# Optimization experiments

Measured on AMD Instinct MI355X. Metric: run time of the kernel, lower is better.

## Reference

```python
import jax, jax.numpy as jnp
import numpy as np

DIM = 256
HEADS = 8
KS = 3          # deform conv kernel size
N = KS * KS     # sampling points per output pixel
PAD = 1


def conv2d(x, w, b=None, stride=1, padding=0):
    out = jax.lax.conv_general_dilated(
        x, w, (stride, stride), [(padding, padding)] * 2,
        dimension_numbers=('NCHW', 'OIHW', 'NCHW'))
    if b is not None:
        out = out + b[None, :, None, None]
    return out


def deform_conv(x, w_pconv, b_pconv, w_dconv):
    b, c, h, w = x.shape
    offset = conv2d(x, w_pconv, b_pconv, padding=1)      # (b, 2N, h, w)
    off = offset.transpose(0, 2, 3, 1)                   # (b, h, w, 2N); [:N]=x-off, [N:]=y-off
    xp = jnp.pad(x, ((0, 0), (0, 0), (PAD, PAD), (PAD, PAD)))
    hp, wp = h + 2 * PAD, w + 2 * PAD
    r = jnp.arange(-(KS - 1) // 2, (KS - 1) // 2 + 1, dtype=x.dtype)
    pnx, pny = jnp.meshgrid(r, r, indexing='ij')
    # sampling positions, 1-indexed into the padded input (matches the torch ref)
    px = off[..., :N] + pnx.reshape(-1) + jnp.arange(1, h + 1, dtype=x.dtype)[None, :, None, None]
    py = off[..., N:] + pny.reshape(-1) + jnp.arange(1, w + 1, dtype=x.dtype)[None, None, :, None]
    fx = jnp.floor(px)
    fy = jnp.floor(py)
    qlt_x = jnp.clip(fx, 0, hp - 1)
    qlt_y = jnp.clip(fy, 0, wp - 1)
    qrb_x = jnp.clip(fx + 1, 0, hp - 1)
    qrb_y = jnp.clip(fy + 1, 0, wp - 1)
    pxc = jnp.clip(px, 0, hp - 1)
    pyc = jnp.clip(py, 0, wp - 1)
    # bilinear weights (can be negative at clamped borders, as in the torch ref)
    g_lt = (1 + (qlt_x - pxc)) * (1 + (qlt_y - pyc))
    g_rb = (1 - (qrb_x - pxc)) * (1 - (qrb_y - pyc))
    g_lb = (1 + (qlt_x - pxc)) * (1 - (qrb_y - pyc))
    g_rt = (1 - (qrb_x - pxc)) * (1 + (qlt_y - pyc))
    ilt_x = qlt_x.astype(jnp.int32)
    ilt_y = qlt_y.astype(jnp.int32)
    irb_x = qrb_x.astype(jnp.int32)
    irb_y = qrb_y.astype(jnp.int32)

    def gather(xb, ix, iy):
        return xb[:, ix, iy]                              # (c, h, w, N)

    gat = jax.vmap(gather)
    x_lt = gat(xp, ilt_x, ilt_y)
    x_rb = gat(xp, irb_x, irb_y)
    x_lb = gat(xp, ilt_x, irb_y)
    x_rt = gat(xp, irb_x, ilt_y)
    x_off = (g_lt[:, None] * x_lt + g_rb[:, None] * x_rb
             + g_lb[:, None] * x_lb + g_rt[:, None] * x_rt)   # (b, c, h, w, N)
    # 'b c h w (i j) -> b c (h i) (w j)' then ks-strided conv
    x_off = x_off.reshape(b, c, h, w, KS, KS).transpose(0, 1, 2, 4, 3, 5)
    x_off = x_off.reshape(b, c, h * KS, w * KS)
    return conv2d(x_off, w_dconv, None, stride=KS)


def ssa_forward(x, w_pconv, b_pconv, w_dconv, w_qkv, temperature, w_proj):
    b, c, h, w = x.shape
    hw = h * w
    ch = c // HEADS
    q = deform_conv(x, w_pconv, b_pconv, w_dconv)         # (b, c, h, w)
    qkv = jnp.einsum('bchw,oc->bohw', x, w_qkv)           # 1x1 conv, (b, 3c, h, w)
    k = qkv[:, c:2 * c]
    v = qkv[:, 2 * c:]
    q = q.reshape(b, HEADS, ch, hw)
    k = k.reshape(b, HEADS, ch, hw)
    v = v.reshape(b, HEADS, ch, hw)
    k = k / jnp.maximum(jnp.linalg.norm(k, axis=-1, keepdims=True), 1e-12)
    v = v / jnp.maximum(jnp.linalg.norm(v, axis=-1, keepdims=True), 1e-12)
    attn = jnp.einsum('bhcn,bhdn->bhcd', q, k) * temperature[None]   # (b, h, ch, ch)
    attn = jax.nn.softmax(attn, axis=-1)
    out = jnp.einsum('bhcd,bhdn->bhcn', attn, v).reshape(b, c, h, w)
    return jnp.einsum('bchw,oc->bohw', out, w_proj)       # project_out 1x1


def setup_inputs() -> dict:
    key = jax.random.key(0)
    ks = jax.random.split(key, 6)
    B, H, W = 2, 96, 96
    x = jax.random.normal(ks[0], (B, DIM, H, W), jnp.float32)
    w_pconv = jax.random.normal(ks[1], (2 * N, DIM, KS, KS), jnp.float32) * 0.01
    b_pconv = jax.random.normal(ks[2], (2 * N,), jnp.float32) * 0.01
    w_dconv = jax.random.normal(ks[3], (DIM, DIM, KS, KS), jnp.float32) * 0.02
    w_qkv = jax.random.normal(ks[4], (3 * DIM, DIM), jnp.float32) * 0.05
    temperature = jnp.ones((HEADS, 1, 1), jnp.float32)
    w_proj = jax.random.normal(ks[5], (DIM, DIM), jnp.float32) * 0.05
    return dict(x=x, w_pconv=w_pconv, b_pconv=b_pconv, w_dconv=w_dconv,
                w_qkv=w_qkv, temperature=temperature, w_proj=w_proj)


def reference(x, w_pconv, b_pconv, w_dconv, w_qkv, temperature, w_proj):
    return ssa_forward(x, w_pconv, b_pconv, w_dconv, w_qkv, temperature, w_proj)
```

## Files before the change

### kernel.cpp

```cpp
#include <hip/hip_runtime.h>
#include <math.h>

#define BB 2
#define CC 256
#define HW 96
#define PP 9216
#define KO 18
#define HEADS 8
#define NCH 36

typedef short bf16x8 __attribute__((ext_vector_type(8)));
typedef float f32x4 __attribute__((ext_vector_type(4)));

#define NP_O    0UL
#define IDX_O   331776UL
#define WGT_O   995328UL
#define WT2_O   1658880UL
#define WP2_O   2248704UL
#define WQ2_O   2322432UL
#define W2_O    2453504UL
#define QP_O    2584576UL
#define KV_O    12021760UL
#define INV_O   21458944UL
#define AP_O    21459968UL
#define AT_O    22049792UL

__device__ __forceinline__ ushort f2bf_rne(float f) {
    unsigned u = __float_as_uint(f);
    unsigned r = (u + 0x7FFFu + ((u >> 16) & 1u)) >> 16;
    return (ushort)r;
}
__device__ __forceinline__ float bf2f(ushort h) {
    return __uint_as_float(((unsigned)h) << 16);
}

__global__ __launch_bounds__(256) void k_prep_wt(const float* __restrict__ wd,
                                                 ushort* __restrict__ h,
                                                 ushort* __restrict__ lo) {
    int tid = blockIdx.x * 256 + threadIdx.x;
    if (tid >= 9 * 8 * 1024 * 8) return;
    int e = tid & 7;
    int u = (tid >> 3) & 1023;
    int cs = (tid >> 13) & 7;
    int kk = tid >> 16;
    int oh = u >> 6, rem = u & 63;
    int lrow = rem & 15, lhi = rem >> 4;
    int o = oh * 16 + lrow;
    int c = cs * 32 + lhi * 8 + e;
    float v = wd[o * 2304 + c * 9 + kk];
    ushort hh = f2bf_rne(v);
    h[tid] = hh;
    lo[tid] = f2bf_rne(v - bf2f(hh));
}

__global__ __launch_bounds__(256) void k_prep_wp(const float* __restrict__ wp,
                                                 ushort* __restrict__ h,
                                                 ushort* __restrict__ lo) {
    int tid = blockIdx.x * 256 + threadIdx.x;
    if (tid >= 9 * 8 * 128 * 8) return;
    int e = tid & 7;
    int u = (tid >> 3) & 127;
    int cs = (tid >> 10) & 7;
    int kk = tid >> 13;
    int mf = u >> 6, rem = u & 63;
    int lrow = rem & 15, lhi = rem >> 4;
    int o = mf * 16 + lrow;
    int c = cs * 32 + lhi * 8 + e;
    float v = (o < KO) ? wp[(o * 256 + c) * 9 + kk] : 0.f;
    ushort hh = f2bf_rne(v);
    h[tid] = hh;
    lo[tid] = f2bf_rne(v - bf2f(hh));
}

__global__ __launch_bounds__(256) void k_prep_w(const float* __restrict__ W,
                                                ushort* __restrict__ h,
                                                ushort* __restrict__ lo,
                                                int total) {
    int tid = blockIdx.x * 256 + threadIdx.x;
    if (tid >= total) return;
    int e = tid & 7;
    int u = (tid >> 3) & 1023;
    int csg = (tid >> 13) & 7;
    int mt = tid >> 16;
    int rem = u & 63;
    int lrow = rem & 15, lhi = rem >> 4;
    int o = mt * 256 + (u >> 6) * 16 + lrow;
    int c = csg * 32 + lhi * 8 + e;
    float v = W[o * 256 + c];
    ushort hh = f2bf_rne(v);
    h[tid] = hh;
    lo[tid] = f2bf_rne(v - bf2f(hh));
}

__global__ __launch_bounds__(256) void k_pconv(const float* __restrict__ x,
                                               const ushort* __restrict__ wp2h,
                                               const ushort* __restrict__ wp2l,
                                               float* __restrict__ ppart) {
    int s = blockIdx.x;
    int xcd = s & 7;
    int b = xcd & 1, ks = xcd >> 1;
    int p0 = (s >> 3) * 64;
    int t = threadIdx.x;
    int l = t & 63, w = t >> 6;
    int lrow = l & 15, lhi = l >> 4;
    int p = t & 63, cg = t >> 6;
    __shared__ __align__(16) ushort Sh[64 * 40];
    __shared__ __align__(16) ushort Sl[64 * 40];
    f32x4 acc[2];
    acc[0] = (f32x4)0.f; acc[1] = (f32x4)0.f;
    const float* xb = x + (size_t)b * CC * PP;
    int pix = p0 + p;
    int i_ = pix / 96, j_ = pix % 96;
#pragma unroll 1
    for (int cs = 0; cs < 2; ++cs) {
        int csg = ks * 2 + cs;
        const float* xc0 = xb + (size_t)(csg * 32 + cg * 8) * PP;
#pragma unroll 1
        for (int kk = 0; kk < 9; ++kk) {
            int di = kk / 3 - 1, dj = kk % 3 - 1;
            bool vOK = ((unsigned)(i_ + di) < 96u) && ((unsigned)(j_ + dj) < 96u);
            int poff = pix + di * 96 + dj;
            __syncthreads();
            bf16x8 ah[2], al[2];
#pragma unroll
            for (int mf = 0; mf < 2; ++mf) {
                size_t gi = (((size_t)(kk * 8 + csg)) * 128 + (mf * 64 + l)) * 8;
                ah[mf] = *(const bf16x8*)&wp2h[gi];
                al[mf] = *(const bf16x8*)&wp2l[gi];
            }
            bf16x8 vh, vl;
#pragma unroll
            for (int i = 0; i < 8; ++i) {
                float v = vOK ? xc0[(size_t)i * PP + poff] : 0.f;
                ushort hh = f2bf_rne(v);
                vh[i] = (short)hh;
                vl[i] = (short)f2bf_rne(v - bf2f(hh));
            }
            *(bf16x8*)&Sh[p * 40 + cg * 8] = vh;
            *(bf16x8*)&Sl[p * 40 + cg * 8] = vl;
            __syncthreads();
            bf16x8 Bh = *(const bf16x8*)&Sh[(w * 16 + lrow) * 40 + lhi * 8];
            bf16x8 Bl = *(const bf16x8*)&Sl[(w * 16 + lrow) * 40 + lhi * 8];
#pragma unroll
            for (int mf = 0; mf < 2; ++mf) {
                acc[mf] = __builtin_amdgcn_mfma_f32_16x16x32_bf16(ah[mf], Bh, acc[mf], 0, 0, 0);
                acc[mf] = __builtin_amdgcn_mfma_f32_16x16x32_bf16(ah[mf], Bl, acc[mf], 0, 0, 0);
                acc[mf] = __builtin_amdgcn_mfma_f32_16x16x32_bf16(al[mf], Bh, acc[mf], 0, 0, 0);
            }
        }
    }
    float* pr = ppart + ((size_t)(ks * BB + b) * 32) * PP;
#pragma unroll
    for (int mf = 0; mf < 2; ++mf)
#pragma unroll
        for (int j = 0; j < 4; ++j)
            pr[(size_t)(mf * 16 + lhi * 4 + j) * PP + p0 + w * 16 + lrow] = acc[mf][j];
}

__global__ __launch_bounds__(256) void k_bilin2(const float* __restrict__ pp,
                                                const float* __restrict__ bp,
                                                int4* __restrict__ idx4,
                                                float4* __restrict__ wgt4) {
    int idx = blockIdx.x * 256 + threadIdx.x;
    if (idx >= BB * 9 * PP) return;
    int p = idx % PP;
    int bn = idx / PP;
    int n = bn % 9, b = bn / 9;
    int i = p / 96, j = p % 96;
    float ox = bp[n], oy = bp[n + 9];
#pragma unroll
    for (int k = 0; k < 4; ++k) {
        ox += pp[((size_t)(k * BB + b) * 32 + n) * PP + p];
        oy += pp[((size_t)(k * BB + b) * 32 + n + 9) * PP + p];
    }
    float px = ox + (float)(n / 3 - 1) + (float)(i + 1);
    float py = oy + (float)(n % 3 - 1) + (float)(j + 1);
    float fx = floorf(px), fy = floorf(py);
    float qltx = fminf(fmaxf(fx, 0.f), 97.f);
    float qlty = fminf(fmaxf(fy, 0.f), 97.f);
    float qrbx = fminf(fmaxf(fx + 1.f, 0.f), 97.f);
    float qrby = fminf(fmaxf(fy + 1.f, 0.f), 97.f);
    float pxc = fminf(fmaxf(px, 0.f), 97.f);
    float pyc = fminf(fmaxf(py, 0.f), 97.f);
    float glt = (1.f + (qltx - pxc)) * (1.f + (qlty - pyc));
    float grb = (1.f - (qrbx - pxc)) * (1.f - (qrby - pyc));
    float glb = (1.f + (qltx - pxc)) * (1.f - (qrby - pyc));
    float grt = (1.f - (qrbx - pxc)) * (1.f + (qlty - pyc));
    int x0 = (int)qltx - 1, y0 = (int)qlty - 1;
    int x1 = (int)qrbx - 1, y1 = (int)qrby - 1;
    bool vlt = (x0 >= 0 && x0 < 96 && y0 >= 0 && y0 < 96);
    bool vrb = (x1 >= 0 && x1 < 96 && y1 >= 0 && y1 < 96);
    bool vlb = (x0 >= 0 && x0 < 96 && y1 >= 0 && y1 < 96);
    bool vrt = (x1 >= 0 && x1 < 96 && y0 >= 0 && y0 < 96);
    int4 id;
    id.x = vlt ? x0 * 96 + y0 : 0;
    id.y = vrb ? x1 * 96 + y1 : 0;
    id.z = vlb ? x0 * 96 + y1 : 0;
    id.w = vrt ? x1 * 96 + y0 : 0;
    idx4[idx] = id;
    wgt4[idx] = make_float4(vlt ? glt : 0.f, vrb ? grb : 0.f,
                            vlb ? glb : 0.f, vrt ? grt : 0.f);
}

__global__ __launch_bounds__(256) void k_dconv(const float* __restrict__ x,
                                               const ushort* __restrict__ wt2h,
                                               const ushort* __restrict__ wt2l,
                                               const int4* __restrict__ idx4,
                                               const float4* __restrict__ wgt4,
                                               float* __restrict__ qpart) {
    int s = blockIdx.x;
    int xcd = s & 7, ib = s >> 3;
    int combo = xcd >> 1;
    int b = combo & 1;
    int half = combo >> 1;
    int p0 = ((xcd & 1) * 72 + ib) * 64;
    int t = threadIdx.x;
    int l = t & 63, w = t >> 6;
    int lrow = l & 15, lhi = l >> 4;
    int obase = w * 64;
    int p = t & 63, cg = t >> 6;

    __shared__ __align__(16) ushort Sh0[64 * 40], Sl0[64 * 40];
    __shared__ __align__(16) ushort Sh1[64 * 40], Sl1[64 * 40];
    __shared__ int4 Tid[9 * 64];
    __shared__ float4 Twg[9 * 64];

    for (int e = t; e < 9 * 64; e += 256) {
        int kk = e >> 6, pl = e & 63;
        size_t tb = ((size_t)b * 9 + kk) * PP + p0 + pl;
        Tid[e] = idx4[tb];
        Twg[e] = wgt4[tb];
    }

    f32x4 acc[4][4];
#pragma unroll
    for (int mf = 0; mf < 4; ++mf)
#pragma unroll
        for (int nf = 0; nf < 4; ++nf) acc[mf][nf] = (f32x4)0.f;

    const float* xb = x + (size_t)b * CC * PP;
    int h4 = half * 4;

    float R[32];
    float4 g4r;

    auto LD = [&](int i) {
        int csg = h4 + i / 9, kk = i % 9;
        int4 id = Tid[kk * 64 + p];
        g4r = Twg[kk * 64 + p];
        const float* xp0 = xb + (size_t)(csg * 32 + cg * 8) * PP;
#pragma unroll
        for (int q = 0; q < 8; ++q) {
            const float* xc = xp0 + (size_t)q * PP;
            R[q * 4 + 0] = xc[id.x];
            R[q * 4 + 1] = xc[id.y];
            R[q * 4 + 2] = xc[id.z];
            R[q * 4 + 3] = xc[id.w];
        }
    };
    auto CONV = [&](ushort* Sh, ushort* Sl) {
        bf16x8 vh, vl;
#pragma unroll
        for (int q = 0; q < 8; ++q) {
            float v = g4r.x * R[q * 4 + 0];
            v = fmaf(g4r.y, R[q * 4 + 1], v);
            v = fmaf(g4r.z, R[q * 4 + 2], v);
            v = fmaf(g4r.w, R[q * 4 + 3], v);
            ushort hh = f2bf_rne(v);
            vh[q] = (short)hh;
            vl[q] = (short)f2bf_rne(v - bf2f(hh));
        }
        *(bf16x8*)&Sh[p * 40 + cg * 8] = vh;
        *(bf16x8*)&Sl[p * 40 + cg * 8] = vl;
    };
    auto COMPUTE = [&](int i, const ushort* Sh, const ushort* Sl) {
        int csg = h4 + i / 9, kk = i % 9;
        bf16x8 ah[4], al[4];
#pragma unroll
        for (int mf = 0; mf < 4; ++mf) {
            size_t gi = (((size_t)(kk * 8 + csg)) * 1024 + ((w * 4 + mf) * 64 + l)) * 8;
            ah[mf] = *(const bf16x8*)&wt2h[gi];
            al[mf] = *(const bf16x8*)&wt2l[gi];
        }
        bf16x8 Bh4[4], Bl4[4];
#pragma unroll
        for (int nf = 0; nf < 4; ++nf) {
            Bh4[nf] = *(const bf16x8*)&Sh[(nf * 16 + lrow) * 40 + lhi * 8];
            Bl4[nf] = *(const bf16x8*)&Sl[(nf * 16 + lrow) * 40 + lhi * 8];
        }
#pragma unroll
        for (int mf = 0; mf < 4; ++mf)
#pragma unroll
            for (int nf = 0; nf < 4; ++nf) {
                acc[mf][nf] = __builtin_amdgcn_mfma_f32_16x16x32_bf16(ah[mf], Bh4[nf], acc[mf][nf], 0, 0, 0);
                acc[mf][nf] = __builtin_amdgcn_mfma_f32_16x16x32_bf16(ah[mf], Bl4[nf], acc[mf][nf], 0, 0, 0);
                acc[mf][nf] = __builtin_amdgcn_mfma_f32_16x16x32_bf16(al[mf], Bh4[nf], acc[mf][nf], 0, 0, 0);
            }
    };

    __syncthreads();
    LD(0); CONV(Sh0, Sl0);
    LD(1);
    __syncthreads();

#pragma unroll 1
    for (int i0 = 0; i0 < 36; i0 += 2) {
        COMPUTE(i0, Sh0, Sl0);
        CONV(Sh1, Sl1);
        if (i0 + 2 < 36) LD(i0 + 2);
        __syncthreads();
        COMPUTE(i0 + 1, Sh1, Sl1);
        if (i0 + 2 < 36) {
            CONV(Sh0, Sl0);
            if (i0 + 3 < 36) LD(i0 + 3);
        }
        __syncthreads();
    }

    float* qh = qpart + (size_t)half * BB * CC * PP + (size_t)b * CC * PP;
#pragma unroll
    for (int mf = 0; mf < 4; ++mf)
#pragma unroll
        for (int nf = 0; nf < 4; ++nf)
#pragma unroll
            for (int j = 0; j < 4; ++j)
                qh[(size_t)(obase + mf * 16 + lhi * 4 + j) * PP + p0 + nf * 16 + lrow] =
                    acc[mf][nf][j];
}

__global__ __launch_bounds__(256) void k_gemm_bf(const float* __restrict__ Bsrc,
                                                 const ushort* __restrict__ A2h,
                                                 const ushort* __restrict__ A2l,
                                                 float* __restrict__ C,
                                                 int mtiles, int bRowStride, int bRowOff,
                                                 int aBatchStride,
                                                 float* __restrict__ npart) {
    int s = blockIdx.x;
    int xcd = s & 7, ib = s >> 3;
    int b, mt, ptile;
    if (mtiles == 2) {
        int combo = xcd >> 1;
        b = combo & 1; mt = combo >> 1;
        ptile = (xcd & 1) * 72 + ib;
    } else {
        b = xcd >> 2; mt = 0;
        ptile = (xcd & 3) * 36 + ib;
    }
    int p0 = ptile * 64;
    int t = threadIdx.x;
    int l = t & 63, w = t >> 6;
    int lrow = l & 15, lhi = l >> 4;
    int obase = w * 64;
    int p = t & 63, cg = t >> 6;
    __shared__ __align__(16) ushort Sh[64 * 40];
    __shared__ __align__(16) ushort Sl[64 * 40];
    f32x4 acc[4][4];
#pragma unroll
    for (int mf = 0; mf < 4; ++mf)
#pragma unroll
        for (int nf = 0; nf < 4; ++nf) acc[mf][nf] = (f32x4)0.f;
    const float* Bb = Bsrc + ((size_t)b * bRowStride + bRowOff) * PP;
    const ushort* Ah = A2h + (size_t)b * aBatchStride;
    const ushort* Al = A2l + (size_t)b * aBatchStride;
#pragma unroll 1
    for (int csg = 0; csg < 8; ++csg) {
        __syncthreads();
        bf16x8 ah[4], al[4];
#pragma unroll
        for (int mf = 0; mf < 4; ++mf) {
            size_t gi = (((size_t)(mt * 8 + csg)) * 1024 + ((w * 4 + mf) * 64 + l)) * 8;
            ah[mf] = *(const bf16x8*)&Ah[gi];
            al[mf] = *(const bf16x8*)&Al[gi];
        }
        const float* xr = Bb + (size_t)(csg * 32 + cg * 8) * PP + p0 + p;
        bf16x8 vh, vl;
#pragma unroll
        for (int i = 0; i < 8; ++i) {
            float v = xr[(size_t)i * PP];
            ushort hh = f2bf_rne(v);
            vh[i] = (short)hh;
            vl[i] = (short)f2bf_rne(v - bf2f(hh));
        }
        *(bf16x8*)&Sh[p * 40 + cg * 8] = vh;
        *(bf16x8*)&Sl[p * 40 + cg * 8] = vl;
        __syncthreads();
        bf16x8 Bh4[4], Bl4[4];
#pragma unroll
        for (int nf = 0; nf < 4; ++nf) {
            Bh4[nf] = *(const bf16x8*)&Sh[(nf * 16 + lrow) * 40 + lhi * 8];
            Bl4[nf] = *(const bf16x8*)&Sl[(nf * 16 + lrow) * 40 + lhi * 8];
        }
#pragma unroll
        for (int mf = 0; mf < 4; ++mf) {
#pragma unroll
            for (int nf = 0; nf < 4; ++nf) {
                acc[mf][nf] = __builtin_amdgcn_mfma_f32_16x16x32_bf16(ah[mf], Bh4[nf], acc[mf][nf], 0, 0, 0);
                acc[mf][nf] = __builtin_amdgcn_mfma_f32_16x16x32_bf16(ah[mf], Bl4[nf], acc[mf][nf], 0, 0, 0);
                acc[mf][nf] = __builtin_amdgcn_mfma_f32_16x16x32_bf16(al[mf], Bh4[nf], acc[mf][nf], 0, 0, 0);
            }
        }
    }
    float* Cb = C + (size_t)b * (mtiles * 256) * PP;
#pragma unroll
    for (int mf = 0; mf < 4; ++mf)
#pragma unroll
        for (int nf = 0; nf < 4; ++nf)
#pragma unroll
            for (int j = 0; j < 4; ++j)
                Cb[(size_t)(mt * 256 + obase + mf * 16 + lhi * 4 + j) * PP + p0 + nf * 16 + lrow] =
                    acc[mf][nf][j];
    if (npart) {
        float sq[4][4];
#pragma unroll
        for (int mf = 0; mf < 4; ++mf)
#pragma unroll
            for (int j = 0; j < 4; ++j) {
                float v0 = acc[mf][0][j], v1 = acc[mf][1][j];
                float v2 = acc[mf][2][j], v3 = acc[mf][3][j];
                sq[mf][j] = v0 * v0 + v1 * v1 + v2 * v2 + v3 * v3;
            }
#pragma unroll
        for (int m = 1; m <= 8; m <<= 1)
#pragma unroll
            for (int mf = 0; mf < 4; ++mf)
#pragma unroll
                for (int j = 0; j < 4; ++j)
                    sq[mf][j] += __shfl_xor(sq[mf][j], m, 64);
        if (lrow == 0) {
            float* np = npart + ((size_t)(b * 2 + mt) * 144 + ptile) * 256;
#pragma unroll
            for (int mf = 0; mf < 4; ++mf)
#pragma unroll
                for (int j = 0; j < 4; ++j)
                    np[obase + mf * 16 + lhi * 4 + j] = sq[mf][j];
        }
    }
}

__global__ __launch_bounds__(256) void k_norm2(const float* __restrict__ np,
                                               float* __restrict__ invn) {
    int r = blockIdx.x * 256 + threadIdx.x;
    if (r >= 1024) return;
    int b = r >> 9, g = r & 511;
    int mt = g >> 8, row = g & 255;
    const float* base = np + ((size_t)(b * 2 + mt) * 144) * 256 + row;
    float s = 0.f;
    for (int pt = 0; pt < 144; ++pt) s += base[pt * 256];
    invn[b * 512 + g] = 1.f / fmaxf(sqrtf(s), 1e-12f);
}

__global__ __launch_bounds__(256) void k_attn_part(const float* __restrict__ qp,
                                                   const float* __restrict__ kv,
                                                   float* __restrict__ apart) {
    int ch = blockIdx.x, h = blockIdx.y, b = blockIdx.z;
    int t = threadIdx.x;
    int d = t & 31, cg = t >> 5;
    __shared__ float qs[32][37], ks[32][37];
    float acc[4] = {0.f, 0.f, 0.f, 0.f};
    const float* q0 = qp + ((size_t)b * CC + h * 32) * PP;
    const float* q1 = q0 + (size_t)BB * CC * PP;
    const float* kb = kv + ((size_t)b * 512 + h * 32) * PP;
    int r = t >> 3, cq = (t & 7) * 4;
    for (int po = ch * 256; po < ch * 256 + 256; po += 32) {
        float4 va = *(const float4*)&q0[(size_t)r * PP + po + cq];
        float4 vb = *(const float4*)&q1[(size_t)r * PP + po + cq];
        qs[r][cq + 0] = va.x + vb.x; qs[r][cq + 1] = va.y + vb.y;
        qs[r][cq + 2] = va.z + vb.z; qs[r][cq + 3] = va.w + vb.w;
        float4 vk = *(const float4*)&kb[(size_t)r * PP + po + cq];
        ks[r][cq + 0] = vk.x; ks[r][cq + 1] = vk.y;
        ks[r][cq + 2] = vk.z; ks[r][cq + 3] = vk.w;
        __syncthreads();
#pragma unroll
        for (int pq = 0; pq < 32; ++pq) {
            float kvv = ks[d][pq];
#pragma unroll
            for (int i = 0; i < 4; ++i)
                acc[i] = fmaf(qs[cg * 4 + i][pq], kvv, acc[i]);
        }
        __syncthreads();
    }
    float* ap = apart + (((size_t)(b * 8 + h) * NCH + ch) << 10);
#pragma unroll
    for (int i = 0; i < 4; ++i) ap[(cg * 4 + i) * 32 + d] = acc[i];
}

__global__ __launch_bounds__(256) void k_attn_fin(const float* __restrict__ apart,
                                                  const float* __restrict__ invn,
                                                  const float* __restrict__ temp,
                                                  float* __restrict__ attns) {
    int h = blockIdx.x, b = blockIdx.y;
    int t = threadIdx.x;
    __shared__ float A[32][33];
    const float* ap = apart + ((size_t)(b * 8 + h) * NCH << 10);
    float th = temp[h];
    for (int e = t; e < 1024; e += 256) {
        float s = 0.f;
        for (int chn = 0; chn < NCH; ++chn) s += ap[chn * 1024 + e];
        int c = e >> 5, d = e & 31;
        A[c][d] = s * th * invn[b * 512 + h * 32 + d];
    }
    __syncthreads();
    if (t < 32) {
        int c = t;
        float m = -INFINITY;
#pragma unroll
        for (int d = 0; d < 32; ++d) m = fmaxf(m, A[c][d]);
        float sum = 0.f;
#pragma unroll
        for (int d = 0; d < 32; ++d) sum += expf(A[c][d] - m);
        float inv = 1.f / sum;
        float* at = attns + ((size_t)(b * 8 + h) << 10) + c * 32;
#pragma unroll
        for (int d = 0; d < 32; ++d)
            at[d] = expf(A[c][d] - m) * inv * invn[b * 512 + 256 + h * 32 + d];
    }
}

__global__ __launch_bounds__(256) void k_w2(const float* __restrict__ attns,
                                            const float* __restrict__ wproj,
                                            ushort* __restrict__ w2h,
                                            ushort* __restrict__ w2l) {
    int h = blockIdx.x, b = blockIdx.y;
    int t = threadIdx.x;
    __shared__ float As[32][33];
    for (int e = t; e < 1024; e += 256)
        As[e >> 5][e & 31] = attns[((size_t)(b * 8 + h) << 10) + e];
    __syncthreads();
    int o = t;
    float wrow[32];
#pragma unroll
    for (int c = 0; c < 32; ++c) wrow[c] = wproj[o * 256 + h * 32 + c];
    int wq = o >> 6, mf = (o >> 4) & 3, lr = o & 15;
    size_t bb = (size_t)b * 65536;
#pragma unroll
    for (int e = 0; e < 32; ++e) {
        float v = 0.f;
#pragma unroll
        for (int c = 0; c < 32; ++c) v = fmaf(wrow[c], As[c][e], v);
        int lhi = e >> 3, ee = e & 7;
        size_t gi = bb + ((size_t)h * 1024 + ((wq * 4 + mf) * 64 + lhi * 16 + lr)) * 8 + ee;
        ushort hh = f2bf_rne(v);
        w2h[gi] = hh;
        w2l[gi] = f2bf_rne(v - bf2f(hh));
    }
}

extern "C" void kernel_launch(void* const* d_in, const int* in_sizes, int n_in,
                              void* d_out, int out_size, void* d_ws, size_t ws_size,
                              hipStream_t stream) {
    const float* x     = (const float*)d_in[0];
    const float* wp    = (const float*)d_in[1];
    const float* bp    = (const float*)d_in[2];
    const float* wd    = (const float*)d_in[3];
    const float* wqkv  = (const float*)d_in[4];
    const float* temp  = (const float*)d_in[5];
    const float* wproj = (const float*)d_in[6];
    float* out = (float*)d_out;
    float* ws  = (float*)d_ws;

    float* npart  = ws + NP_O;
    int4*  idx4   = (int4*)(ws + IDX_O);
    float4* wgt4  = (float4*)(ws + WGT_O);
    ushort* wt2h  = (ushort*)(ws + WT2_O);
    ushort* wt2l  = wt2h + 9 * 8 * 1024 * 8;
    ushort* wp2h  = (ushort*)(ws + WP2_O);
    ushort* wp2l  = wp2h + 9 * 8 * 128 * 8;
    ushort* wq2h  = (ushort*)(ws + WQ2_O);
    ushort* wq2l  = wq2h + 2 * 8 * 1024 * 8;
    ushort* w2h   = (ushort*)(ws + W2_O);
    ushort* w2l   = w2h + 2 * 65536;
    float* qpart  = ws + QP_O;
    float* ppart  = ws + QP_O;
    float* kv     = ws + KV_O;
    float* invn   = ws + INV_O;
    float* apart  = ws + AP_O;
    float* attns  = ws + AT_O;

    k_prep_wt<<<2304, 256, 0, stream>>>(wd, wt2h, wt2l);
    k_prep_wp<<<288, 256, 0, stream>>>(wp, wp2h, wp2l);
    k_prep_w<<<512, 256, 0, stream>>>(wqkv + 256 * 256, wq2h, wq2l, 2 * 65536);
    k_pconv<<<1152, 256, 0, stream>>>(x, wp2h, wp2l, ppart);
    k_bilin2<<<(BB * 9 * PP + 255) / 256, 256, 0, stream>>>(ppart, bp, idx4, wgt4);
    k_dconv<<<576, 256, 0, stream>>>(x, wt2h, wt2l, idx4, wgt4, qpart);
    k_gemm_bf<<<576, 256, 0, stream>>>(x, wq2h, wq2l, kv, 2, 256, 0, 0, npart);
    k_norm2<<<4, 256, 0, stream>>>(npart, invn);
    k_attn_part<<<dim3(NCH, HEADS, BB), 256, 0, stream>>>(qpart, kv, apart);
    k_attn_fin<<<dim3(HEADS, BB), 256, 0, stream>>>(apart, invn, temp, attns);
    k_w2<<<dim3(HEADS, BB), 256, 0, stream>>>(attns, wproj, w2h, w2l);
    k_gemm_bf<<<288, 256, 0, stream>>>(kv, w2h, w2l, out, 1, 512, 256, 65536, nullptr);
}
```

Baseline: 319.3 us.

## Stage dconv weight tiles into LDS via async global_load_lds

The deformable-conv GEMM kernel now copies each 16 KB hi/lo bf16 weight tile into shared memory with direct global-to-LDS loads, so the MFMA loop reads A fragments from LDS instead of global memory. The double-buffered B staging is replaced by a single buffer, and the loop becomes one iteration per K-chunk with the next gather load issued before the compute. This aims to cut global-load latency on the weight operand, but it loses the previous two-deep software pipeline and adds a barrier per chunk. There is no explicit wait on the async LDS loads beyond __syncthreads, so correctness depends on the compiler inserting vmcnt waits.

```diff
diff --git a/kernel.cpp b/kernel.cpp
--- a/kernel.cpp
+++ b/kernel.cpp
@@ -32,6 +32,10 @@
 }
 __device__ __forceinline__ float bf2f(ushort h) {
     return __uint_as_float(((unsigned)h) << 16);
+}
+__device__ __forceinline__ void gload_lds16(const void* g, void* l) {
+    __builtin_amdgcn_global_load_lds((const __attribute__((address_space(1))) void*)g,
+                                     (__attribute__((address_space(3))) void*)l, 16, 0, 0);
 }
 
 __global__ __launch_bounds__(256) void k_prep_wt(const float* __restrict__ wd,
@@ -220,8 +224,8 @@
     int obase = w * 64;
     int p = t & 63, cg = t >> 6;
 
-    __shared__ __align__(16) ushort Sh0[64 * 40], Sl0[64 * 40];
-    __shared__ __align__(16) ushort Sh1[64 * 40], Sl1[64 * 40];
+    __shared__ __align__(16) ushort Ah_l[8192], Al_l[8192];
+    __shared__ __align__(16) ushort Sh[64 * 40], Sl[64 * 40];
     __shared__ int4 Tid[9 * 64];
     __shared__ float4 Twg[9 * 64];
 
@@ -244,6 +248,21 @@
     float R[32];
     float4 g4r;
 
+    auto ISSUE_A = [&](int i) {
+        int csg = h4 + i / 9, kk = i % 9;
+        const ushort* gh = wt2h + ((size_t)(kk * 8 + csg)) * 8192;
+        const ushort* gl = wt2l + ((size_t)(kk * 8 + csg)) * 8192;
+#pragma unroll
+        for (int r = 0; r < 4; ++r) {
+            int u = r * 256 + t;
+            gload_lds16(gh + (size_t)u * 8, &Ah_l[u * 8]);
+        }
+#pragma unroll
+        for (int r = 0; r < 4; ++r) {
+            int u = r * 256 + t;
+            gload_lds16(gl + (size_t)u * 8, &Al_l[u * 8]);
+        }
+    };
     auto LD = [&](int i) {
         int csg = h4 + i / 9, kk = i % 9;
         int4 id = Tid[kk * 64 + p];
@@ -258,7 +277,7 @@
             R[q * 4 + 3] = xc[id.w];
         }
     };
-    auto CONV = [&](ushort* Sh, ushort* Sl) {
+    auto CONV = [&]() {
         bf16x8 vh, vl;
 #pragma unroll
         for (int q = 0; q < 8; ++q) {
@@ -273,14 +292,12 @@
         *(bf16x8*)&Sh[p * 40 + cg * 8] = vh;
         *(bf16x8*)&Sl[p * 40 + cg * 8] = vl;
     };
-    auto COMPUTE = [&](int i, const ushort* Sh, const ushort* Sl) {
-        int csg = h4 + i / 9, kk = i % 9;
+    auto COMPUTE = [&]() {
         bf16x8 ah[4], al[4];
 #pragma unroll
         for (int mf = 0; mf < 4; ++mf) {
-            size_t gi = (((size_t)(kk * 8 + csg)) * 1024 + ((w * 4 + mf) * 64 + l)) * 8;
-            ah[mf] = *(const bf16x8*)&wt2h[gi];
-            al[mf] = *(const bf16x8*)&wt2l[gi];
+            ah[mf] = *(const bf16x8*)&Ah_l[((w * 4 + mf) * 64 + l) * 8];
+            al[mf] = *(const bf16x8*)&Al_l[((w * 4 + mf) * 64 + l) * 8];
         }
         bf16x8 Bh4[4], Bl4[4];
 #pragma unroll
@@ -298,22 +315,16 @@
             }
     };
 
+    LD(0);
     __syncthreads();
-    LD(0); CONV(Sh0, Sl0);
-    LD(1);
-    __syncthreads();
 
 #pragma unroll 1
-    for (int i0 = 0; i0 < 36; i0 += 2) {
-        COMPUTE(i0, Sh0, Sl0);
-        CONV(Sh1, Sl1);
-        if (i0 + 2 < 36) LD(i0 + 2);
+    for (int i = 0; i < 36; ++i) {
+        ISSUE_A(i);
+        CONV();
         __syncthreads();
-        COMPUTE(i0 + 1, Sh1, Sl1);
-        if (i0 + 2 < 36) {
-            CONV(Sh0, Sl0);
-            if (i0 + 3 < 36) LD(i0 + 3);
-        }
+        if (i + 1 < 36) LD(i + 1);
+        COMPUTE();
         __syncthreads();
     }
 
```

New measurement: 327.6 us. +2.6%, slower.

## Halve deform-conv pixel tile to 32 and reorder gather/MFMA pipeline

Applied to the files above, without the earlier changes.

The deformable conv kernel now processes 32 pixels per block instead of 64 and launches twice as many blocks (1152). Per-thread gather registers and accumulators are halved, so occupancy should rise and the grid should fill the GPU better. The loop is reordered so the next tile's gathers are issued before the MFMA compute, and s_setprio raises wave priority during the MFMA burst to overlap memory latency with math. In exchange, each weight fragment loaded from global memory is reused over half as many pixels, which doubles weight traffic per output.

```diff
diff --git a/kernel.cpp b/kernel.cpp
--- a/kernel.cpp
+++ b/kernel.cpp
@@ -213,44 +213,46 @@
     int combo = xcd >> 1;
     int b = combo & 1;
     int half = combo >> 1;
-    int p0 = ((xcd & 1) * 72 + ib) * 64;
+    int ptile = (xcd & 1) * 144 + ib;
+    int p0 = ptile * 32;
     int t = threadIdx.x;
     int l = t & 63, w = t >> 6;
     int lrow = l & 15, lhi = l >> 4;
     int obase = w * 64;
-    int p = t & 63, cg = t >> 6;
-
-    __shared__ __align__(16) ushort Sh0[64 * 40], Sl0[64 * 40];
-    __shared__ __align__(16) ushort Sh1[64 * 40], Sl1[64 * 40];
-    __shared__ int4 Tid[9 * 64];
-    __shared__ float4 Twg[9 * 64];
-
-    for (int e = t; e < 9 * 64; e += 256) {
-        int kk = e >> 6, pl = e & 63;
-        size_t tb = ((size_t)b * 9 + kk) * PP + p0 + pl;
+    int pl = t & 31, cg = t >> 5;
+
+    __shared__ __align__(16) ushort Sh0[32 * 40], Sl0[32 * 40];
+    __shared__ __align__(16) ushort Sh1[32 * 40], Sl1[32 * 40];
+    __shared__ int4 Tid[9 * 32];
+    __shared__ float4 Twg[9 * 32];
+
+    for (int e = t; e < 9 * 32; e += 256) {
+        int kk = e >> 5, pq = e & 31;
+        size_t tb = ((size_t)b * 9 + kk) * PP + p0 + pq;
         Tid[e] = idx4[tb];
         Twg[e] = wgt4[tb];
     }
 
-    f32x4 acc[4][4];
+    f32x4 acc[4][2];
 #pragma unroll
     for (int mf = 0; mf < 4; ++mf)
 #pragma unroll
-        for (int nf = 0; nf < 4; ++nf) acc[mf][nf] = (f32x4)0.f;
+        for (int nf = 0; nf < 2; ++nf) acc[mf][nf] = (f32x4)0.f;
 
     const float* xb = x + (size_t)b * CC * PP;
     int h4 = half * 4;
 
-    float R[32];
+    float R[16];
     float4 g4r;
 
     auto LD = [&](int i) {
-        int csg = h4 + i / 9, kk = i % 9;
-        int4 id = Tid[kk * 64 + p];
-        g4r = Twg[kk * 64 + p];
-        const float* xp0 = xb + (size_t)(csg * 32 + cg * 8) * PP;
-#pragma unroll
-        for (int q = 0; q < 8; ++q) {
+        int cs = i / 9, kk = i % 9;
+        int csg = h4 + cs;
+        int4 id = Tid[kk * 32 + pl];
+        g4r = Twg[kk * 32 + pl];
+        const float* xp0 = xb + (size_t)(csg * 32 + cg * 4) * PP;
+#pragma unroll
+        for (int q = 0; q < 4; ++q) {
             const float* xc = xp0 + (size_t)q * PP;
             R[q * 4 + 0] = xc[id.x];
             R[q * 4 + 1] = xc[id.y];
@@ -259,22 +261,26 @@
         }
     };
     auto CONV = [&](ushort* Sh, ushort* Sl) {
-        bf16x8 vh, vl;
-#pragma unroll
-        for (int q = 0; q < 8; ++q) {
+        ushort4 vh, vl;
+#pragma unroll
+        for (int q = 0; q < 4; ++q) {
             float v = g4r.x * R[q * 4 + 0];
             v = fmaf(g4r.y, R[q * 4 + 1], v);
             v = fmaf(g4r.z, R[q * 4 + 2], v);
             v = fmaf(g4r.w, R[q * 4 + 3], v);
             ushort hh = f2bf_rne(v);
-            vh[q] = (short)hh;
-            vl[q] = (short)f2bf_rne(v - bf2f(hh));
-        }
-        *(bf16x8*)&Sh[p * 40 + cg * 8] = vh;
-        *(bf16x8*)&Sl[p * 40 + cg * 8] = vl;
+            ushort ll = f2bf_rne(v - bf2f(hh));
+            if (q == 0)      { vh.x = hh; vl.x = ll; }
+            else if (q == 1) { vh.y = hh; vl.y = ll; }
+            else if (q == 2) { vh.z = hh; vl.z = ll; }
+            else             { vh.w = hh; vl.w = ll; }
+        }
+        *(ushort4*)&Sh[pl * 40 + cg * 4] = vh;
+        *(ushort4*)&Sl[pl * 40 + cg * 4] = vl;
     };
     auto COMPUTE = [&](int i, const ushort* Sh, const ushort* Sl) {
-        int csg = h4 + i / 9, kk = i % 9;
+        int cs = i / 9, kk = i % 9;
+        int csg = h4 + cs;
         bf16x8 ah[4], al[4];
 #pragma unroll
         for (int mf = 0; mf < 4; ++mf) {
@@ -282,20 +288,22 @@
             ah[mf] = *(const bf16x8*)&wt2h[gi];
             al[mf] = *(const bf16x8*)&wt2l[gi];
         }
-        bf16x8 Bh4[4], Bl4[4];
-#pragma unroll
-        for (int nf = 0; nf < 4; ++nf) {
-            Bh4[nf] = *(const bf16x8*)&Sh[(nf * 16 + lrow) * 40 + lhi * 8];
-            Bl4[nf] = *(const bf16x8*)&Sl[(nf * 16 + lrow) * 40 + lhi * 8];
-        }
+        bf16x8 Bh2[2], Bl2[2];
+#pragma unroll
+        for (int nf = 0; nf < 2; ++nf) {
+            Bh2[nf] = *(const bf16x8*)&Sh[(nf * 16 + lrow) * 40 + lhi * 8];
+            Bl2[nf] = *(const bf16x8*)&Sl[(nf * 16 + lrow) * 40 + lhi * 8];
+        }
+        __builtin_amdgcn_s_setprio(1);
 #pragma unroll
         for (int mf = 0; mf < 4; ++mf)
 #pragma unroll
-            for (int nf = 0; nf < 4; ++nf) {
-                acc[mf][nf] = __builtin_amdgcn_mfma_f32_16x16x32_bf16(ah[mf], Bh4[nf], acc[mf][nf], 0, 0, 0);
-                acc[mf][nf] = __builtin_amdgcn_mfma_f32_16x16x32_bf16(ah[mf], Bl4[nf], acc[mf][nf], 0, 0, 0);
-                acc[mf][nf] = __builtin_amdgcn_mfma_f32_16x16x32_bf16(al[mf], Bh4[nf], acc[mf][nf], 0, 0, 0);
+            for (int nf = 0; nf < 2; ++nf) {
+                acc[mf][nf] = __builtin_amdgcn_mfma_f32_16x16x32_bf16(ah[mf], Bh2[nf], acc[mf][nf], 0, 0, 0);
+                acc[mf][nf] = __builtin_amdgcn_mfma_f32_16x16x32_bf16(ah[mf], Bl2[nf], acc[mf][nf], 0, 0, 0);
+                acc[mf][nf] = __builtin_amdgcn_mfma_f32_16x16x32_bf16(al[mf], Bh2[nf], acc[mf][nf], 0, 0, 0);
             }
+        __builtin_amdgcn_s_setprio(0);
     };
 
     __syncthreads();
@@ -305,15 +313,13 @@
 
 #pragma unroll 1
     for (int i0 = 0; i0 < 36; i0 += 2) {
-        COMPUTE(i0, Sh0, Sl0);
         CONV(Sh1, Sl1);
         if (i0 + 2 < 36) LD(i0 + 2);
+        COMPUTE(i0, Sh0, Sl0);
         __syncthreads();
+        if (i0 + 2 < 36) CONV(Sh0, Sl0);
+        if (i0 + 3 < 36) LD(i0 + 3);
         COMPUTE(i0 + 1, Sh1, Sl1);
-        if (i0 + 2 < 36) {
-            CONV(Sh0, Sl0);
-            if (i0 + 3 < 36) LD(i0 + 3);
-        }
         __syncthreads();
     }
 
@@ -321,7 +327,7 @@
 #pragma unroll
     for (int mf = 0; mf < 4; ++mf)
 #pragma unroll
-        for (int nf = 0; nf < 4; ++nf)
+        for (int nf = 0; nf < 2; ++nf)
 #pragma unroll
             for (int j = 0; j < 4; ++j)
                 qh[(size_t)(obase + mf * 16 + lhi * 4 + j) * PP + p0 + nf * 16 + lrow] =
@@ -581,7 +587,7 @@
     k_prep_w<<<512, 256, 0, stream>>>(wqkv + 256 * 256, wq2h, wq2l, 2 * 65536);
     k_pconv<<<1152, 256, 0, stream>>>(x, wp2h, wp2l, ppart);
     k_bilin2<<<(BB * 9 * PP + 255) / 256, 256, 0, stream>>>(ppart, bp, idx4, wgt4);
-    k_dconv<<<576, 256, 0, stream>>>(x, wt2h, wt2l, idx4, wgt4, qpart);
+    k_dconv<<<1152, 256, 0, stream>>>(x, wt2h, wt2l, idx4, wgt4, qpart);
     k_gemm_bf<<<576, 256, 0, stream>>>(x, wq2h, wq2l, kv, 2, 256, 0, 0, npart);
     k_norm2<<<4, 256, 0, stream>>>(npart, invn);
     k_attn_part<<<dim3(NCH, HEADS, BB), 256, 0, stream>>>(qpart, kv, apart);
```

Result: faster. 299.5 us (-6.2%).
